# Kernel optimization log

Hardware: AMD Instinct MI355X
Metric: run time of the kernel (lower is better)

Reference implementation:

```python
import jax, jax.numpy as jnp
import numpy as np

# Static config derived from img size 144 (min spatial dim > 128 branch):
SCALES = [9, 18, 36]            # kernel sizes (cubic)
WEIGHTS = [0.1, 0.3, 0.6]       # kernel weight ratios
DILATIONS = [2, 2, 2]
STRIDES = [max((k + 1) // 4, 1) for k in SCALES]  # [2, 4, 9]
EPS = 1e-5


def _box_sum(x, k, stride, dil):
    # Local sum over a dilated k^3 window, valid padding (matches F.conv3d
    # with an all-ones [1,1,k,k,k] kernel).
    kern = jnp.ones((1, 1, k, k, k), dtype=x.dtype)
    return jax.lax.conv_general_dilated(
        x, kern,
        window_strides=(stride,) * 3,
        padding='VALID',
        rhs_dilation=(dil,) * 3,
        dimension_numbers=('NCDHW', 'OIDHW', 'NCDHW'))


def setup_inputs() -> dict:
    key = jax.random.key(0)
    k1, k2 = jax.random.split(key)
    shape = (4, 1, 144, 144, 144)
    return {
        'input': jax.random.normal(k1, shape, dtype=jnp.float32),
        'target': jax.random.normal(k2, shape, dtype=jnp.float32),
    }


def reference(input, target):
    B = input.shape[0]
    input_2 = input * input
    target_2 = target * target
    input_target = input * target
    lncc_total = jnp.float32(0.0)
    for k, w, dil, st in zip(SCALES, WEIGHTS, DILATIONS, STRIDES):
        i_sum = _box_sum(input, k, st, dil).reshape(B, -1)
        t_sum = _box_sum(target, k, st, dil).reshape(B, -1)
        i2_sum = _box_sum(input_2, k, st, dil).reshape(B, -1)
        t2_sum = _box_sum(target_2, k, st, dil).reshape(B, -1)
        it_sum = _box_sum(input_target, k, st, dil).reshape(B, -1)
        numel = float(k ** 3)
        i_mean = i_sum / numel
        t_mean = t_sum / numel
        cross = it_sum - t_mean * i_sum - i_mean * t_sum + t_mean * i_mean * numel
        i_var = i2_sum - 2.0 * i_mean * i_sum + i_mean * i_mean * numel
        t_var = t2_sum - 2.0 * t_mean * t_sum + t_mean * t_mean * numel
        lncc = (cross * cross) / (i_var * t_var + EPS)
        lncc_total = lncc_total + w * (1.0 - lncc.mean())
    return lncc_total * B
```

## Files before the change

kernel.cpp:

```cpp
#include <hip/hip_runtime.h>


constexpr int BATCH = 4;
constexpr int DIM   = 144;
constexpr int NROWS = BATCH * DIM * DIM;
constexpr float EPS = 1e-5f;

constexpr int N1C  = NROWS * 9;
constexpr int N2Ae = BATCH * 72 * 64 * 64;
constexpr int N2Be = BATCH * 72 * 28 * 28;
constexpr int N2C  = BATCH * DIM * 9 * 9;


__device__ __forceinline__ float lncc_val(const float s[5], float inv_numel) {
    float cross = s[4] - s[0] * s[1] * inv_numel;
    float ivar  = s[2] - s[0] * s[0] * inv_numel;
    float tvar  = s[3] - s[1] * s[1] * inv_numel;
    return (cross * cross) / (ivar * tvar + EPS);
}

__device__ __forceinline__ void block_reduce_store(float acc, float* slot) {
    #pragma unroll
    for (int off = 32; off > 0; off >>= 1) acc += __shfl_down(acc, off, 64);
    __shared__ float sm[4];
    int lane = threadIdx.x & 63, wid = threadIdx.x >> 6;
    if (lane == 0) sm[wid] = acc;
    __syncthreads();
    if (threadIdx.x == 0) *slot = sm[0] + sm[1] + sm[2] + sm[3];
}


__device__ void aXY_body(int blk, const float* __restrict__ in,
                         const float* __restrict__ tg,
                         float* __restrict__ b2a, float* xs)
{
    const int p  = blk >> 2;
    const int c  = blk & 3;
    const int b  = p / 72;
    const int ez = p % 72;
    const int xo0 = c * 16;
    const size_t gpl = (size_t)(b * DIM + 2 * ez) * (DIM * DIM);
    const int t = threadIdx.x;

    for (int i = t; i < 72 * 16; i += 256) {
        int yp = i >> 4, dx = i & 15;
        size_t g = gpl + (size_t)(2 * yp) * DIM + 2 * (size_t)(xo0 + dx);
        const float* ga = in + g;
        const float* gb = tg + g;
        float s0 = 0.f, s1 = 0.f, s2 = 0.f, s3 = 0.f, s4 = 0.f;
        #pragma unroll
        for (int j = 0; j < 9; ++j) {
            float a = ga[2 * j], bb = gb[2 * j];
            s0 += a; s1 += bb; s2 += a * a; s3 += bb * bb; s4 += a * bb;
        }
        float* d = &xs[yp * 81 + dx];
        d[0] = s0; d[16] = s1; d[32] = s2; d[48] = s3; d[64] = s4;
    }
    __syncthreads();

    for (int it = t; it < 320; it += 256) {
        int dx = it & 15;
        int q  = (it >> 4) % 5;
        int ch = it / 80;
        int yo0 = ch << 4;
        const float* xp = &xs[q * 16 + dx];
        float s = 0.f;
        #pragma unroll
        for (int j = 0; j < 9; ++j) s += xp[(yo0 + j) * 81];
        float* ob = b2a + (size_t)q * N2Ae + ((size_t)p * 64 + yo0) * 64 + xo0 + dx;
        ob[0] = s;
        #pragma unroll
        for (int i2 = 1; i2 < 16; ++i2) {
            s += xp[(yo0 + i2 + 8) * 81] - xp[(yo0 + i2 - 1) * 81];
            ob[(size_t)i2 * 64] = s;
        }
    }
}

constexpr int CXROWS = 12;

__device__ void cX_body(int blk, const float* __restrict__ in,
                        const float* __restrict__ tg,
                        float* __restrict__ b1c, float* sm)
{
    float* la = sm;
    float* lb = sm + CXROWS * 145;
    const int t = threadIdx.x;
    const int row0 = blk * CXROWS;
    const float* gin = in + (size_t)row0 * DIM;
    const float* gtg = tg + (size_t)row0 * DIM;
    for (int i = t; i < CXROWS * DIM; i += 256) {
        int rr = i / DIM, cc = i % DIM;
        la[rr * 145 + cc] = gin[i];
        lb[rr * 145 + cc] = gtg[i];
    }
    __syncthreads();
    if (t < CXROWS * 18) {
        int rr  = t / 18;
        int rem = t % 18;
        int xo = rem >> 1, sp = rem & 1;
        const float* pa = &la[rr * 145 + xo * 9 + 2 * sp];
        const float* pb = &lb[rr * 145 + xo * 9 + 2 * sp];
        float s0 = 0.f, s1 = 0.f, s2 = 0.f, s3 = 0.f, s4 = 0.f;
        #pragma unroll
        for (int jj = 0; jj < 18; ++jj) {
            float a = pa[4 * jj], b = pb[4 * jj];
            s0 += a; s1 += b; s2 += a * a; s3 += b * b; s4 += a * b;
        }
        s0 += __shfl_xor(s0, 1, 64);
        s1 += __shfl_xor(s1, 1, 64);
        s2 += __shfl_xor(s2, 1, 64);
        s3 += __shfl_xor(s3, 1, 64);
        s4 += __shfl_xor(s4, 1, 64);
        if (sp == 0) {
            int o = (row0 + rr) * 9 + xo;
            b1c[o] = s0; b1c[N1C + o] = s1; b1c[2 * N1C + o] = s2;
            b1c[3 * N1C + o] = s3; b1c[4 * N1C + o] = s4;
        }
    }
}

constexpr int B_AXY = BATCH * 72 * 4;
constexpr int B_CX  = NROWS / CXROWS;
constexpr int SM1   = 72 * 81;

__global__ __launch_bounds__(256) void k1(const float* __restrict__ in,
                                          const float* __restrict__ tg,
                                          float* __restrict__ b2a,
                                          float* __restrict__ b1c)
{
    __shared__ float smem[SM1];
    int blk = blockIdx.x;
    if (blk < B_AXY) aXY_body(blk, in, tg, b2a, smem);
    else             cX_body(blk - B_AXY, in, tg, b1c, smem);
}


__device__ __forceinline__ void aZ_body(int blk, const float* __restrict__ b2a,
                                        float* __restrict__ pA)
{
    int tid = blk * 256 + threadIdx.x;
    float acc = 0.f;
    {
        int xo = tid & 63;
        int yo = (tid >> 6) & 63;
        int ch = (tid >> 12) & 7;
        int b  = tid >> 15;
        const int zo0 = ch * 8;
        const int OO = 64 * 64;
        const float* base = b2a + (size_t)b * 72 * OO + yo * 64 + xo;

        float s[5] = {0.f, 0.f, 0.f, 0.f, 0.f};
        #pragma unroll
        for (int j = 0; j < 9; ++j) {
            #pragma unroll
            for (int q = 0; q < 5; ++q)
                s[q] += base[(size_t)q * N2Ae + (zo0 + j) * OO];
        }
        acc += lncc_val(s, 1.0f / 729.0f);
        #pragma unroll
        for (int i = 1; i < 8; ++i) {
            #pragma unroll
            for (int q = 0; q < 5; ++q)
                s[q] += base[(size_t)q * N2Ae + (zo0 + i + 8) * OO]
                      - base[(size_t)q * N2Ae + (zo0 + i - 1) * OO];
            acc += lncc_val(s, 1.0f / 729.0f);
        }
    }
    block_reduce_store(acc, pA + blk);
}

__device__ __forceinline__ void bXY_body(int tid, const float* __restrict__ b2a,
                                         float* __restrict__ b2b)
{
    const int total = BATCH * 72 * 28 * 28;
    if (tid >= total) return;
    int xo = tid % 28;
    int yo = (tid / 28) % 28;
    int p  = tid / 784;
    const float* ib = b2a + (size_t)p * 4096;
    float* ob = b2b + (size_t)p * 784 + yo * 28 + xo;
    int r0 = (2 * yo) * 64 + 2 * xo;
    #pragma unroll
    for (int q = 0; q < 5; ++q) {
        const float* pq = ib + (size_t)q * N2Ae;
        ob[(size_t)q * N2Be] =
            pq[r0] + pq[r0 + 9] + pq[r0 + 9 * 64] + pq[r0 + 9 * 64 + 9];
    }
}

__device__ __forceinline__ void cY_body(int tid, const float* __restrict__ b1c,
                                        float* __restrict__ b2c)
{
    const int total = BATCH * DIM * 9 * 9 * 8;
    if (tid >= total) return;
    int sp   = tid & 7;
    int rest = tid >> 3;
    int xo = rest % 9;
    int yo = (rest / 9) % 9;
    int bz = rest / 81;
    const float* base = b1c + (size_t)bz * DIM * 9 + xo;

    float s[5] = {0.f, 0.f, 0.f, 0.f, 0.f};
    #pragma unroll
    for (int j = 0; j < 36; ++j) {
        if ((j & 7) == sp) {
            int y = 9 * yo + 2 * j;
            #pragma unroll
            for (int q = 0; q < 5; ++q) s[q] += base[(size_t)q * N1C + y * 9];
        }
    }
    #pragma unroll
    for (int off = 1; off < 8; off <<= 1) {
        #pragma unroll
        for (int q = 0; q < 5; ++q) s[q] += __shfl_xor(s[q], off, 64);
    }
    if (sp == 0) {
        float* ob = b2c + (size_t)bz * 81 + yo * 9 + xo;
        #pragma unroll
        for (int q = 0; q < 5; ++q) ob[(size_t)q * N2C] = s[q];
    }
}

constexpr int B_AZ  = (BATCH * 8 * 64 * 64) / 256;
constexpr int B_BXY = (BATCH * 72 * 28 * 28) / 256;
constexpr int B_CY  = (BATCH * DIM * 9 * 9 * 8) / 256;

__global__ __launch_bounds__(256) void k2(const float* __restrict__ b2a,
                                          const float* __restrict__ b1c,
                                          float* __restrict__ b2b,
                                          float* __restrict__ b2c,
                                          float* __restrict__ pA)
{
    int blk = blockIdx.x;
    if (blk < B_AZ)              aZ_body(blk, b2a, pA);
    else if (blk < B_AZ + B_BXY) bXY_body((blk - B_AZ) * 256 + threadIdx.x, b2a, b2b);
    else                         cY_body((blk - B_AZ - B_BXY) * 256 + threadIdx.x, b1c, b2c);
}


__device__ __forceinline__ void bZ_body(int blk, const float* __restrict__ b2b,
                                        float* __restrict__ pB)
{
    int tid = blk * 256 + threadIdx.x;
    float acc = 0.f;
    {
        int sp   = tid & 7;
        int rest = tid >> 3;
        int xo = rest % 28;
        int yo = (rest / 28) % 28;
        int zo = (rest / 784) % 28;
        int b  = rest / 21952;
        const int OO = 784;
        const float* base = b2b + (size_t)b * 72 * OO + yo * 28 + xo;

        float s[5] = {0.f, 0.f, 0.f, 0.f, 0.f};
        #pragma unroll
        for (int j = 0; j < 18; ++j) {
            if ((j & 7) == sp) {
                #pragma unroll
                for (int q = 0; q < 5; ++q)
                    s[q] += base[(size_t)q * N2Be + (2 * zo + j) * OO];
            }
        }
        #pragma unroll
        for (int off = 1; off < 8; off <<= 1) {
            #pragma unroll
            for (int q = 0; q < 5; ++q) s[q] += __shfl_xor(s[q], off, 64);
        }
        if (sp == 0) acc = lncc_val(s, 1.0f / 5832.0f);
    }
    block_reduce_store(acc, pB + blk);
}

__device__ __forceinline__ void cZ_body(int blk, const float* __restrict__ b2c,
                                        float* __restrict__ pC)
{
    int tid = blk * 256 + threadIdx.x;
    const int total = BATCH * 9 * 9 * 9 * 16;
    float acc = 0.f;
    if (tid < total) {
        int sp   = tid & 15;
        int rest = tid >> 4;
        int xo = rest % 9;
        int yo = (rest / 9) % 9;
        int zo = (rest / 81) % 9;
        int b  = rest / 729;
        const int OO = 81;
        const float* base = b2c + (size_t)b * DIM * OO + yo * 9 + xo;

        float s[5] = {0.f, 0.f, 0.f, 0.f, 0.f};
        #pragma unroll
        for (int j = 0; j < 36; ++j) {
            if ((j & 15) == sp) {
                int z = 9 * zo + 2 * j;
                #pragma unroll
                for (int q = 0; q < 5; ++q) s[q] += base[(size_t)q * N2C + z * OO];
            }
        }
        #pragma unroll
        for (int off = 1; off < 16; off <<= 1) {
            #pragma unroll
            for (int q = 0; q < 5; ++q) s[q] += __shfl_xor(s[q], off, 64);
        }
        if (sp == 0) acc = lncc_val(s, 1.0f / 46656.0f);
    }
    block_reduce_store(acc, pC + blk);
}

constexpr int B_BZ = (BATCH * 28 * 28 * 28 * 8) / 256;
constexpr int B_CZ = (BATCH * 9 * 9 * 9 * 16 + 255) / 256;

__global__ __launch_bounds__(256) void k3(const float* __restrict__ b2b,
                                          const float* __restrict__ b2c,
                                          float* __restrict__ pB,
                                          float* __restrict__ pC)
{
    int blk = blockIdx.x;
    if (blk < B_BZ) bZ_body(blk, b2b, pB);
    else            cZ_body(blk - B_BZ, b2c, pC);
}


__global__ __launch_bounds__(256) void k4(const float* __restrict__ pA,
                                          const float* __restrict__ pB,
                                          const float* __restrict__ pC,
                                          float* __restrict__ out)
{
    const int t = threadIdx.x;
    float sA = 0.f, sB = 0.f, sC = 0.f;
    for (int i = t; i < B_AZ; i += 256) sA += pA[i];
    for (int i = t; i < B_BZ; i += 256) sB += pB[i];
    for (int i = t; i < B_CZ; i += 256) sC += pC[i];
    float s = (0.1f / 262144.0f) * sA + (0.3f / 21952.0f) * sB
            + (0.6f / 729.0f) * sC;
    #pragma unroll
    for (int off = 32; off > 0; off >>= 1) s += __shfl_down(s, off, 64);
    __shared__ float sm[4];
    int lane = t & 63, wid = t >> 6;
    if (lane == 0) sm[wid] = s;
    __syncthreads();
    if (t == 0) out[0] = 4.0f - (sm[0] + sm[1] + sm[2] + sm[3]);
}

extern "C" void kernel_launch(void* const* d_in, const int* in_sizes, int n_in,
                              void* d_out, int out_size, void* d_ws, size_t ws_size,
                              hipStream_t stream) {
    const float* input  = (const float*)d_in[0];
    const float* target = (const float*)d_in[1];
    float* out = (float*)d_out;

    float* b2a = (float*)d_ws;
    float* b1c = b2a + (size_t)5 * N2Ae;
    float* b2b = b1c + (size_t)5 * N1C;
    float* b2c = b2b + (size_t)5 * N2Be;
    float* pA  = b2c + (size_t)5 * N2C;
    float* pB  = pA + B_AZ;
    float* pC  = pB + B_BZ;

    k1<<<B_AXY + B_CX, 256, 0, stream>>>(input, target, b2a, b1c);
    k2<<<B_AZ + B_BXY + B_CY, 256, 0, stream>>>(b2a, b1c, b2b, b2c, pA);
    k3<<<B_BZ + B_CZ, 256, 0, stream>>>(b2b, b2c, pB, pC);
    k4<<<1, 256, 0, stream>>>(pA, pB, pC, out);
}
```

Baseline: 88.16 us.

## Vectorize first-stage loads and interleave input/target in shared memory

The XY-pass body now has each thread load float4 vectors covering two adjacent outputs, keep the stride-2 elements in registers, and write paired float2 partial sums. The vertical pass then works on float2 pairs, so half as many threads are active. The X-pass body loads rows as float4, interleaves input and target into one padded shared buffer, and doubles the rows per block, which removes the shuffle-based split of each window sum. The aim is fewer global load instructions and fewer LDS accesses, at the cost of loading every other element unused and higher register use per thread.

```diff
diff --git a/kernel.cpp b/kernel.cpp
--- a/kernel.cpp
+++ b/kernel.cpp
@@ -42,87 +42,105 @@
     const size_t gpl = (size_t)(b * DIM + 2 * ez) * (DIM * DIM);
     const int t = threadIdx.x;
 
-    for (int i = t; i < 72 * 16; i += 256) {
-        int yp = i >> 4, dx = i & 15;
-        size_t g = gpl + (size_t)(2 * yp) * DIM + 2 * (size_t)(xo0 + dx);
-        const float* ga = in + g;
-        const float* gb = tg + g;
-        float s0 = 0.f, s1 = 0.f, s2 = 0.f, s3 = 0.f, s4 = 0.f;
+    for (int i = t; i < 576; i += 256) {
+        int yp = i >> 3, dp = i & 7;
+        int dx0 = dp * 2;
+        int e0  = xo0 + dx0;
+        const float* rowa = in + gpl + (size_t)(2 * yp) * DIM;
+        const float* rowb = tg + gpl + (size_t)(2 * yp) * DIM;
+        const float4* ga = (const float4*)rowa + (e0 >> 1);
+        const float4* gb = (const float4*)rowb + (e0 >> 1);
+        float ea[10], eb[10];
+        #pragma unroll
+        for (int k = 0; k < 5; ++k) {
+            float4 A = ga[k]; ea[2 * k] = A.x; ea[2 * k + 1] = A.z;
+            float4 B = gb[k]; eb[2 * k] = B.x; eb[2 * k + 1] = B.z;
+        }
+        float* xr = &xs[yp * 82 + dx0];
+        #pragma unroll
+        for (int q = 0; q < 5; ++q) {
+            float2 sq; sq.x = 0.f; sq.y = 0.f;
+            #pragma unroll
+            for (int j = 0; j < 9; ++j) {
+                float a0 = ea[j],     b0 = eb[j];
+                float a1 = ea[j + 1], b1 = eb[j + 1];
+                float v0, v1;
+                if (q == 0)      { v0 = a0;      v1 = a1; }
+                else if (q == 1) { v0 = b0;      v1 = b1; }
+                else if (q == 2) { v0 = a0 * a0; v1 = a1 * a1; }
+                else if (q == 3) { v0 = b0 * b0; v1 = b1 * b1; }
+                else             { v0 = a0 * b0; v1 = a1 * b1; }
+                sq.x += v0; sq.y += v1;
+            }
+            *(float2*)&xr[q * 16] = sq;
+        }
+    }
+    __syncthreads();
+
+    if (t < 160) {
+        int dp = t & 7;
+        int q  = (t >> 3) % 5;
+        int ch = t / 40;
+        int dx0 = 2 * dp, yo0 = ch * 16;
+        const float2* xp2 = (const float2*)xs + ((q * 16 + dx0) >> 1);
+        float2 s; s.x = 0.f; s.y = 0.f;
         #pragma unroll
         for (int j = 0; j < 9; ++j) {
-            float a = ga[2 * j], bb = gb[2 * j];
-            s0 += a; s1 += bb; s2 += a * a; s3 += bb * bb; s4 += a * bb;
-        }
-        float* d = &xs[yp * 81 + dx];
-        d[0] = s0; d[16] = s1; d[32] = s2; d[48] = s3; d[64] = s4;
-    }
-    __syncthreads();
-
-    for (int it = t; it < 320; it += 256) {
-        int dx = it & 15;
-        int q  = (it >> 4) % 5;
-        int ch = it / 80;
-        int yo0 = ch << 4;
-        const float* xp = &xs[q * 16 + dx];
-        float s = 0.f;
-        #pragma unroll
-        for (int j = 0; j < 9; ++j) s += xp[(yo0 + j) * 81];
-        float* ob = b2a + (size_t)q * N2Ae + ((size_t)p * 64 + yo0) * 64 + xo0 + dx;
+            float2 v = xp2[(yo0 + j) * 41];
+            s.x += v.x; s.y += v.y;
+        }
+        float2* ob = (float2*)(b2a + (size_t)q * N2Ae
+                               + ((size_t)p * 64 + yo0) * 64 + xo0 + dx0);
         ob[0] = s;
         #pragma unroll
         for (int i2 = 1; i2 < 16; ++i2) {
-            s += xp[(yo0 + i2 + 8) * 81] - xp[(yo0 + i2 - 1) * 81];
-            ob[(size_t)i2 * 64] = s;
-        }
-    }
-}
-
-constexpr int CXROWS = 12;
+            float2 vn = xp2[(yo0 + i2 + 8) * 41];
+            float2 vo = xp2[(yo0 + i2 - 1) * 41];
+            s.x += vn.x - vo.x; s.y += vn.y - vo.y;
+            ob[(size_t)i2 * 32] = s;
+        }
+    }
+}
+
+constexpr int CXROWS   = 24;
+constexpr int CXSTRIDE = 292;
 
 __device__ void cX_body(int blk, const float* __restrict__ in,
                         const float* __restrict__ tg,
-                        float* __restrict__ b1c, float* sm)
-{
-    float* la = sm;
-    float* lb = sm + CXROWS * 145;
+                        float* __restrict__ b1c, float* lv)
+{
     const int t = threadIdx.x;
     const int row0 = blk * CXROWS;
-    const float* gin = in + (size_t)row0 * DIM;
-    const float* gtg = tg + (size_t)row0 * DIM;
-    for (int i = t; i < CXROWS * DIM; i += 256) {
-        int rr = i / DIM, cc = i % DIM;
-        la[rr * 145 + cc] = gin[i];
-        lb[rr * 145 + cc] = gtg[i];
+    const float4* gin = (const float4*)(in + (size_t)row0 * DIM);
+    const float4* gtg = (const float4*)(tg + (size_t)row0 * DIM);
+    for (int i4 = t; i4 < CXROWS * 36; i4 += 256) {
+        int rr = i4 / 36, k = i4 % 36;
+        float4 A = gin[i4], B = gtg[i4];
+        float4* d = (float4*)&lv[rr * CXSTRIDE + k * 8];
+        float4 w0; w0.x = A.x; w0.y = B.x; w0.z = A.y; w0.w = B.y;
+        float4 w1; w1.x = A.z; w1.y = B.z; w1.z = A.w; w1.w = B.w;
+        d[0] = w0; d[1] = w1;
     }
     __syncthreads();
-    if (t < CXROWS * 18) {
-        int rr  = t / 18;
-        int rem = t % 18;
-        int xo = rem >> 1, sp = rem & 1;
-        const float* pa = &la[rr * 145 + xo * 9 + 2 * sp];
-        const float* pb = &lb[rr * 145 + xo * 9 + 2 * sp];
+    if (t < CXROWS * 9) {
+        int rr = t / 9, xo = t % 9;
+        const float2* pp = (const float2*)&lv[rr * CXSTRIDE] + xo * 9;
         float s0 = 0.f, s1 = 0.f, s2 = 0.f, s3 = 0.f, s4 = 0.f;
         #pragma unroll
-        for (int jj = 0; jj < 18; ++jj) {
-            float a = pa[4 * jj], b = pb[4 * jj];
-            s0 += a; s1 += b; s2 += a * a; s3 += b * b; s4 += a * b;
-        }
-        s0 += __shfl_xor(s0, 1, 64);
-        s1 += __shfl_xor(s1, 1, 64);
-        s2 += __shfl_xor(s2, 1, 64);
-        s3 += __shfl_xor(s3, 1, 64);
-        s4 += __shfl_xor(s4, 1, 64);
-        if (sp == 0) {
-            int o = (row0 + rr) * 9 + xo;
-            b1c[o] = s0; b1c[N1C + o] = s1; b1c[2 * N1C + o] = s2;
-            b1c[3 * N1C + o] = s3; b1c[4 * N1C + o] = s4;
-        }
+        for (int j = 0; j < 36; ++j) {
+            float2 ab = pp[2 * j];
+            float a = ab.x, bb = ab.y;
+            s0 += a; s1 += bb; s2 += a * a; s3 += bb * bb; s4 += a * bb;
+        }
+        int o = (row0 + rr) * 9 + xo;
+        b1c[o] = s0; b1c[N1C + o] = s1; b1c[2 * N1C + o] = s2;
+        b1c[3 * N1C + o] = s3; b1c[4 * N1C + o] = s4;
     }
 }
 
 constexpr int B_AXY = BATCH * 72 * 4;
 constexpr int B_CX  = NROWS / CXROWS;
-constexpr int SM1   = 72 * 81;
+constexpr int SM1   = CXROWS * CXSTRIDE;
 
 __global__ __launch_bounds__(256) void k1(const float* __restrict__ in,
                                           const float* __restrict__ tg,
```

Result: no change. 88.17 us (+0.0%).
